# Optimization experiments

Hardware: AMD Instinct MI355X
Metric: run time of the kernel (lower is better)

Reference implementation:

```python
import jax, jax.numpy as jnp
import numpy as np

B, T, U = 4, 256, 64
D_ENC = D_PRED = 512
JOINT = 1024
VOCAB = 1024


def setup_inputs() -> dict:
    key = jax.random.key(0)
    ks = jax.random.split(key, 8)
    s = lambda d: 1.0 / np.sqrt(d)
    return {
        "enc": jax.random.normal(ks[0], (B, T, D_ENC), jnp.float32),
        "pred": jax.random.normal(ks[1], (B, U, D_PRED), jnp.float32),
        "W_enc": jax.random.normal(ks[2], (D_ENC, JOINT), jnp.float32) * s(D_ENC),
        "b_enc": jnp.zeros((JOINT,), jnp.float32),
        "W_pred": jax.random.normal(ks[3], (D_PRED, JOINT), jnp.float32) * s(D_PRED),
        "b_pred": jnp.zeros((JOINT,), jnp.float32),
        "W_out": jax.random.normal(ks[4], (JOINT, VOCAB), jnp.float32) * s(JOINT),
        "b_out": jnp.zeros((VOCAB,), jnp.float32),
    }


def reference(enc, pred, W_enc, b_enc, W_pred, b_pred, W_out, b_out):
    # Dense projections to joint_dim
    enc_out = jnp.einsum("btd,dj->btj", enc, W_enc) + b_enc      # [B,T,J]
    pred_out = jnp.einsum("bud,dj->buj", pred, W_pred) + b_pred  # [B,U,J]
    # Broadcast add over (T,U), tanh, then vocab projection
    joint = jnp.tanh(enc_out[:, :, None, :] + pred_out[:, None, :, :])  # [B,T,U,J]
    logits = jnp.einsum("btuj,jv->btuv", joint, W_out) + b_out           # [B,T,U,V]
    return logits
```

## Files before the change

### kernel.cpp

```cpp
#include <hip/hip_runtime.h>
#include <hip/hip_bf16.h>


typedef __bf16 bf16x8 __attribute__((ext_vector_type(8)));
typedef float f32x4 __attribute__((ext_vector_type(4)));
typedef unsigned int u32x4 __attribute__((ext_vector_type(4)));
using bf16_t = __hip_bfloat16;

#define B_ 4
#define T_ 256
#define U_ 64
#define DE 512
#define JD 1024
#define VV 1024

__device__ __forceinline__ void gl2lds16(const void* g, void* l) {
  __builtin_amdgcn_global_load_lds(
      (__attribute__((address_space(1))) void*)(g),
      (__attribute__((address_space(3))) void*)(l), 16, 0, 0);
}

__device__ __forceinline__ float fast_tanh(float x) {
  float xx = fminf(fmaxf(x, -30.f), 30.f);
  float e = __expf(2.f * xx);
  return 1.f - 2.f * __builtin_amdgcn_rcpf(e + 1.f);
}

__global__ void cvt_bf16_k(const float* __restrict__ src, bf16_t* __restrict__ dst, int n) {
  int i = (blockIdx.x * blockDim.x + threadIdx.x) * 4;
  if (i >= n) return;
  f32x4 v = *(const f32x4*)(src + i);
  bf16_t o[4];
#pragma unroll
  for (int z = 0; z < 4; ++z) o[z] = __float2bfloat16(v[z]);
  *(unsigned long long*)(dst + i) = *(unsigned long long*)o;
}

__global__ void transpose_cvt_k(const float* __restrict__ src, bf16_t* __restrict__ dst,
                                int K, int N) {
  __shared__ float tile[32][33];
  int nt = blockIdx.x * 32, kt = blockIdx.y * 32;
  int tx = threadIdx.x, ty = threadIdx.y;
#pragma unroll
  for (int i = 0; i < 4; ++i)
    tile[ty + i * 8][tx] = src[(size_t)(kt + ty + i * 8) * N + nt + tx];
  __syncthreads();
#pragma unroll
  for (int i = 0; i < 4; ++i)
    dst[(size_t)(nt + ty + i * 8) * K + kt + tx] = __float2bfloat16(tile[tx][ty + i * 8]);
}

__global__ __launch_bounds__(256) void tanh_mat_k(
    const float* __restrict__ enc_o,
    const float* __restrict__ pred_o,
    bf16_t* __restrict__ joint) {
  size_t i = ((size_t)blockIdx.x * 256 + threadIdx.x) * 8;
  const int m = (int)(i >> 10);
  const int j = (int)(i & 1023);
  const int enc_row  = m >> 6;
  const int pred_row = ((m >> 14) << 6) | (m & 63);
  const f32x4* pe = (const f32x4*)(enc_o  + (size_t)enc_row  * JD + j);
  const f32x4* pp = (const f32x4*)(pred_o + (size_t)pred_row * JD + j);
  bf16_t vals[8];
#pragma unroll
  for (int q = 0; q < 2; ++q) {
    f32x4 e = pe[q], p = pp[q];
#pragma unroll
    for (int z = 0; z < 4; ++z)
      vals[q * 4 + z] = __float2bfloat16(fast_tanh(e[z] + p[z]));
  }
  *(u32x4*)(void*)(joint + i) = *(const u32x4*)(const void*)vals;
}

__global__ __launch_bounds__(256) void proj_gemm_k(
    const bf16_t* __restrict__ A, const bf16_t* __restrict__ Bt,
    const float* __restrict__ bias, float* __restrict__ C, int M, int N, int K) {
  __shared__ bf16_t sA[128 * 32];
  __shared__ bf16_t sB[128 * 32];
  const int tid = threadIdx.x;
  const int wave = tid >> 6, lane = tid & 63;
  const int wm = wave >> 1, wn = wave & 1;
  const int m0 = blockIdx.y * 128, n0 = blockIdx.x * 128;

  f32x4 acc[4][4] = {};

  for (int k0 = 0; k0 < K; k0 += 32) {
    __syncthreads();
#pragma unroll
    for (int r = 0; r < 2; ++r) {
      const int base = (wave + 4 * r) * 1024;
      const int row  = (base >> 6) + (lane >> 2);
      const int kel  = (lane & 3) * 8;
      gl2lds16(A  + (size_t)(m0 + row) * K + k0 + kel, (char*)sA + base);
      gl2lds16(Bt + (size_t)(n0 + row) * K + k0 + kel, (char*)sB + base);
    }
    __syncthreads();
    bf16x8 af[4], bfr[4];
    const int kq = (lane >> 4) * 8;
#pragma unroll
    for (int i = 0; i < 4; ++i) {
      af[i]  = *(const bf16x8*)(const void*)(sA + (wm * 64 + i * 16 + (lane & 15)) * 32 + kq);
      bfr[i] = *(const bf16x8*)(const void*)(sB + (wn * 64 + i * 16 + (lane & 15)) * 32 + kq);
    }
#pragma unroll
    for (int i = 0; i < 4; ++i)
#pragma unroll
      for (int j = 0; j < 4; ++j)
        acc[i][j] = __builtin_amdgcn_mfma_f32_16x16x32_bf16(af[i], bfr[j], acc[i][j], 0, 0, 0);
  }

  float bv[4];
#pragma unroll
  for (int j = 0; j < 4; ++j) bv[j] = bias[n0 + wn * 64 + j * 16 + (lane & 15)];
#pragma unroll
  for (int i = 0; i < 4; ++i) {
    const int row = m0 + wm * 64 + i * 16 + ((lane >> 4) << 2);
#pragma unroll
    for (int j = 0; j < 4; ++j) {
      const int col = n0 + wn * 64 + j * 16 + (lane & 15);
#pragma unroll
      for (int rr = 0; rr < 4; ++rr)
        C[(size_t)(row + rr) * N + col] = acc[i][j][rr] + bv[j];
    }
  }
}

__global__ __launch_bounds__(256) void joint_gemm_k(
    const float* __restrict__ enc_out,
    const float* __restrict__ pred_out,
    const bf16_t* __restrict__ Wt,
    const float* __restrict__ b_out,
    float* __restrict__ out) {
  __shared__ bf16_t sA[128 * 32];
  __shared__ bf16_t sB[128 * 32];
  const int tid = threadIdx.x;
  const int wave = tid >> 6, lane = tid & 63;
  const int wm = wave >> 1, wn = wave & 1;
  const int m0 = blockIdx.y * 128, n0 = blockIdx.x * 128;

  const int ar  = tid >> 1;
  const int ac0 = (tid & 1) * 16;
  const int m = m0 + ar;
  const int enc_row  = m >> 6;
  const int pred_row = ((m >> 14) << 6) | (m & 63);
  const float* pe_base = enc_out  + (size_t)enc_row  * JD + ac0;
  const float* pp_base = pred_out + (size_t)pred_row * JD + ac0;

  f32x4 acc[4][4] = {};

  for (int k0 = 0; k0 < JD; k0 += 32) {
    __syncthreads();
#pragma unroll
    for (int r = 0; r < 2; ++r) {
      const int base = (wave + 4 * r) * 1024;
      const int row  = (base >> 6) + (lane >> 2);
      const int kel  = (lane & 3) * 8;
      gl2lds16(Wt + (size_t)(n0 + row) * JD + k0 + kel, (char*)sB + base);
    }
    bf16_t vals[16];
    const f32x4* pe = (const f32x4*)(pe_base + k0);
    const f32x4* pp = (const f32x4*)(pp_base + k0);
#pragma unroll
    for (int q = 0; q < 4; ++q) {
      f32x4 e = pe[q], p = pp[q];
#pragma unroll
      for (int z = 0; z < 4; ++z)
        vals[q * 4 + z] = __float2bfloat16(fast_tanh(e[z] + p[z]));
    }
    u32x4* dstp = (u32x4*)(void*)((char*)sA + ar * 64 + ac0 * 2);
    dstp[0] = ((const u32x4*)(const void*)vals)[0];
    dstp[1] = ((const u32x4*)(const void*)vals)[1];
    __syncthreads();

    bf16x8 af[4], bfr[4];
    const int kq = (lane >> 4) * 8;
#pragma unroll
    for (int i = 0; i < 4; ++i) {
      af[i]  = *(const bf16x8*)(const void*)(sA + (wm * 64 + i * 16 + (lane & 15)) * 32 + kq);
      bfr[i] = *(const bf16x8*)(const void*)(sB + (wn * 64 + i * 16 + (lane & 15)) * 32 + kq);
    }
#pragma unroll
    for (int i = 0; i < 4; ++i)
#pragma unroll
      for (int j = 0; j < 4; ++j)
        acc[i][j] = __builtin_amdgcn_mfma_f32_16x16x32_bf16(af[i], bfr[j], acc[i][j], 0, 0, 0);
  }

  float bv[4];
#pragma unroll
  for (int j = 0; j < 4; ++j) bv[j] = b_out[n0 + wn * 64 + j * 16 + (lane & 15)];
#pragma unroll
  for (int i = 0; i < 4; ++i) {
    const int row = m0 + wm * 64 + i * 16 + ((lane >> 4) << 2);
#pragma unroll
    for (int j = 0; j < 4; ++j) {
      const int col = n0 + wn * 64 + j * 16 + (lane & 15);
#pragma unroll
      for (int rr = 0; rr < 4; ++rr)
        out[(size_t)(row + rr) * VV + col] = acc[i][j][rr] + bv[j];
    }
  }
}

extern "C" void kernel_launch(void* const* d_in, const int* in_sizes, int n_in,
                              void* d_out, int out_size, void* d_ws, size_t ws_size,
                              hipStream_t stream) {
  const float* enc    = (const float*)d_in[0];
  const float* pred   = (const float*)d_in[1];
  const float* W_enc  = (const float*)d_in[2];
  const float* b_enc  = (const float*)d_in[3];
  const float* W_pred = (const float*)d_in[4];
  const float* b_pred = (const float*)d_in[5];
  const float* W_out  = (const float*)d_in[6];
  const float* b_out  = (const float*)d_in[7];
  float* out = (float*)d_out;

  char* ws = (char*)d_ws;
  bf16_t* encb   = (bf16_t*)(ws + 0x000000);
  bf16_t* predb  = (bf16_t*)(ws + 0x100000);
  bf16_t* WtE    = (bf16_t*)(ws + 0x140000);
  bf16_t* WtP    = (bf16_t*)(ws + 0x240000);
  bf16_t* WtO    = (bf16_t*)(ws + 0x340000);
  float*  enc_o  = (float*) (ws + 0x540000);
  float*  pred_o = (float*) (ws + 0x940000);
  bf16_t* joint  = (bf16_t*)(ws + 0xA40000);
  const size_t WS_NEEDED = 0xA40000 + (size_t)(B_*T_*U_) * JD * sizeof(bf16_t);

  cvt_bf16_k<<<(B_*T_*DE) / 1024, 256, 0, stream>>>(enc, encb, B_*T_*DE);
  cvt_bf16_k<<<(B_*U_*DE) / 1024, 256, 0, stream>>>(pred, predb, B_*U_*DE);
  transpose_cvt_k<<<dim3(JD/32, DE/32), dim3(32, 8), 0, stream>>>(W_enc, WtE, DE, JD);
  transpose_cvt_k<<<dim3(JD/32, DE/32), dim3(32, 8), 0, stream>>>(W_pred, WtP, DE, JD);
  transpose_cvt_k<<<dim3(VV/32, JD/32), dim3(32, 8), 0, stream>>>(W_out, WtO, JD, VV);

  proj_gemm_k<<<dim3(JD/128, (B_*T_)/128), 256, 0, stream>>>(encb, WtE, b_enc, enc_o, B_*T_, JD, DE);
  proj_gemm_k<<<dim3(JD/128, (B_*U_)/128), 256, 0, stream>>>(predb, WtP, b_pred, pred_o, B_*U_, JD, DE);

  if (ws_size >= WS_NEEDED) {
    tanh_mat_k<<<(B_*T_*U_) * JD / (8 * 256), 256, 0, stream>>>(enc_o, pred_o, joint);
    proj_gemm_k<<<dim3(VV/128, (B_*T_*U_)/128), 256, 0, stream>>>(joint, WtO, b_out, out,
                                                                  B_*T_*U_, VV, JD);
  } else {
    joint_gemm_k<<<dim3(VV/128, (B_*T_*U_)/128), 256, 0, stream>>>(enc_o, pred_o, WtO, b_out, out);
  }
}
```

Measured before the change: 517.0 us.

## Replace vocab GEMM with 256x256-tile 8-wave double-buffered MFMA kernel

Adds a dedicated vocab-projection GEMM that uses 256x256 output tiles with 512 threads (8 waves). It double-buffers K-slices in LDS via direct global-to-LDS loads with an XOR swizzle to avoid bank conflicts, and remaps workgroup IDs to group tiles for L2 locality. The aim is more data reuse per loaded byte and overlap of loads with MFMA work in the dominant 16384x1024x1024 GEMM. In exchange, register pressure rises (128 accumulator floats per lane) and occupancy is limited by 64KB of LDS per block.

Result: faster. 473.9 us (-8.3%).

```diff
diff --git a/kernel.cpp b/kernel.cpp
--- a/kernel.cpp
+++ b/kernel.cpp
@@ -125,6 +125,111 @@
   }
 }
 
+
+__device__ __forceinline__ void stage_vtile(const bf16_t* __restrict__ A,
+                                            const bf16_t* __restrict__ Bt,
+                                            int m0, int n0, int k0,
+                                            char* buf, int wave, int lane) {
+  char* ab = buf;
+  char* bb = buf + 16384;
+  const int rw = lane >> 2;
+  const int cl = lane & 3;
+#pragma unroll
+  for (int g = 0; g < 2; ++g) {
+    const int r  = g * 128 + wave * 16 + rw;
+    const int cg = cl ^ ((r >> 1) & 3);
+    gl2lds16(A  + (size_t)(m0 + r) * JD + k0 + cg * 8, ab + (g * 128 + wave * 16) * 64);
+    gl2lds16(Bt + (size_t)(n0 + r) * JD + k0 + cg * 8, bb + (g * 128 + wave * 16) * 64);
+  }
+}
+
+__global__ __launch_bounds__(512, 2) void vocab_gemm8_k(
+    const bf16_t* __restrict__ A,
+    const bf16_t* __restrict__ Bt,
+    const float* __restrict__ bias,
+    float* __restrict__ C) {
+  __shared__ char smem[65536];
+  const int tid  = threadIdx.x;
+  const int wave = tid >> 6, lane = tid & 63;
+  const int wm = wave >> 2, wn = wave & 3;
+
+  const int nwg = gridDim.x;
+  const int cpx = nwg >> 3;
+  const int b   = blockIdx.x;
+  const int lb  = (b & 7) * cpx + (b >> 3);
+  const int n0  = (lb & 3) * 256;
+  const int m0  = (lb >> 2) * 256;
+
+  f32x4 acc[8][4] = {};
+
+  const int NT = JD / 32;
+  stage_vtile(A, Bt, m0, n0, 0,  smem,         wave, lane);
+  stage_vtile(A, Bt, m0, n0, 32, smem + 32768, wave, lane);
+  asm volatile("s_waitcnt vmcnt(4)" ::: "memory");
+  __builtin_amdgcn_s_barrier();
+  __builtin_amdgcn_sched_barrier(0);
+
+  for (int t = 0; t < NT; ++t) {
+    const char* ab = smem + (t & 1) * 32768;
+    const char* bb = ab + 16384;
+    const int kq = lane >> 4;
+
+    bf16x8 bfr[4];
+#pragma unroll
+    for (int j = 0; j < 4; ++j) {
+      const int rb = wn * 64 + j * 16 + (lane & 15);
+      const int cb = kq ^ ((rb >> 1) & 3);
+      bfr[j] = *(const bf16x8*)(const void*)(bb + rb * 64 + cb * 16);
+    }
+#pragma unroll
+    for (int mh = 0; mh < 2; ++mh) {
+      bf16x8 af[4];
+#pragma unroll
+      for (int i = 0; i < 4; ++i) {
+        const int ra = wm * 128 + mh * 64 + i * 16 + (lane & 15);
+        const int ca = kq ^ ((ra >> 1) & 3);
+        af[i] = *(const bf16x8*)(const void*)(ab + ra * 64 + ca * 16);
+      }
+      __builtin_amdgcn_s_setprio(1);
+#pragma unroll
+      for (int i = 0; i < 4; ++i)
+#pragma unroll
+        for (int j = 0; j < 4; ++j)
+          acc[mh * 4 + i][j] =
+              __builtin_amdgcn_mfma_f32_16x16x32_bf16(af[i], bfr[j], acc[mh * 4 + i][j], 0, 0, 0);
+      __builtin_amdgcn_s_setprio(0);
+    }
+
+    if (t + 1 < NT) {
+      __builtin_amdgcn_sched_barrier(0);
+      __builtin_amdgcn_s_barrier();
+      if (t + 2 < NT) {
+        stage_vtile(A, Bt, m0, n0, (t + 2) * 32, smem + (t & 1) * 32768, wave, lane);
+        asm volatile("s_waitcnt vmcnt(4)" ::: "memory");
+      } else {
+        asm volatile("s_waitcnt vmcnt(0)" ::: "memory");
+      }
+      __builtin_amdgcn_s_barrier();
+      __builtin_amdgcn_sched_barrier(0);
+    }
+  }
+
+  float bv[4];
+#pragma unroll
+  for (int j = 0; j < 4; ++j) bv[j] = bias[n0 + wn * 64 + j * 16 + (lane & 15)];
+#pragma unroll
+  for (int i = 0; i < 8; ++i) {
+    const int row = m0 + wm * 128 + i * 16 + ((lane >> 4) << 2);
+#pragma unroll
+    for (int j = 0; j < 4; ++j) {
+      const int col = n0 + wn * 64 + j * 16 + (lane & 15);
+#pragma unroll
+      for (int rr = 0; rr < 4; ++rr)
+        C[(size_t)(row + rr) * VV + col] = acc[i][j][rr] + bv[j];
+    }
+  }
+}
+
 __global__ __launch_bounds__(256) void joint_gemm_k(
     const float* __restrict__ enc_out,
     const float* __restrict__ pred_out,
@@ -237,8 +342,8 @@
 
   if (ws_size >= WS_NEEDED) {
     tanh_mat_k<<<(B_*T_*U_) * JD / (8 * 256), 256, 0, stream>>>(enc_o, pred_o, joint);
-    proj_gemm_k<<<dim3(VV/128, (B_*T_*U_)/128), 256, 0, stream>>>(joint, WtO, b_out, out,
-                                                                  B_*T_*U_, VV, JD);
+    vocab_gemm8_k<<<dim3(((B_*T_*U_) / 256) * (VV / 256)), 512, 0, stream>>>(
+        joint, WtO, b_out, out);
   } else {
     joint_gemm_k<<<dim3(VV/128, (B_*T_*U_)/128), 256, 0, stream>>>(enc_o, pred_o, WtO, b_out, out);
   }
```
